# Optimization experiments

Hardware: AMD Instinct MI355X
Metric: run time of the kernel (lower is better)

## Reference

```python
import jax, jax.numpy as jnp
import numpy as np


def setup_inputs() -> dict:
    key = jax.random.key(0)
    ks = jax.random.split(key, 9)
    B, S, H = 4096, 64, 128
    scale = 0.05
    return {
        "feature_input": jax.random.normal(ks[0], (B, S, H), dtype=jnp.float32),
        "W1": jax.random.normal(ks[1], (S, H, H), dtype=jnp.float32) * scale,
        "b1": jax.random.normal(ks[2], (S, H), dtype=jnp.float32) * scale,
        "W3": jax.random.normal(ks[3], (S, H, H), dtype=jnp.float32) * scale,
        "b3": jax.random.normal(ks[4], (S, H), dtype=jnp.float32) * scale,
        "W_ih": jax.random.normal(ks[5], (3 * H, H), dtype=jnp.float32) * scale,
        "b_ih": jax.random.normal(ks[6], (3 * H,), dtype=jnp.float32) * scale,
        "W_hh": jax.random.normal(ks[7], (3 * H, H), dtype=jnp.float32) * scale,
        "b_hh": jax.random.normal(ks[8], (3 * H,), dtype=jnp.float32) * scale,
    }


def _gru_cell(x, h, W_ih, b_ih, W_hh, b_hh):
    # torch.nn.GRUCell math; gate order in weights is (r, z, n)
    gi = x @ W_ih.T + b_ih  # [N, 3H]
    gh = h @ W_hh.T + b_hh  # [N, 3H]
    H = h.shape[-1]
    gi_r, gi_z, gi_n = gi[:, :H], gi[:, H:2 * H], gi[:, 2 * H:]
    gh_r, gh_z, gh_n = gh[:, :H], gh[:, H:2 * H], gh[:, 2 * H:]
    r = jax.nn.sigmoid(gi_r + gh_r)
    z = jax.nn.sigmoid(gi_z + gh_z)
    n = jnp.tanh(gi_n + r * gh_n)
    return (1.0 - z) * n + z * h


def reference(feature_input, W1, b1, W3, b3, W_ih, b_ih, W_hh, b_hh):
    B, S, H = feature_input.shape
    # message pass: per-sen linear (batched over S as one einsum)
    state1 = jnp.einsum('bsh,soh->bso', feature_input, W1) + b1  # [B,S,H]
    # sum over sentences, broadcast-subtract own contribution
    state2 = jnp.sum(state1, axis=1, keepdims=True) - state1      # [B,S,H]
    state3 = jnp.einsum('bsh,soh->bso', state2, W3) + b3          # [B,S,H]
    # GRU cell update over flattened (B*S) nodes
    h_new = _gru_cell(state3.reshape(-1, H), feature_input.reshape(-1, H),
                      W_ih, b_ih, W_hh, b_hh)
    return feature_input + h_new.reshape(B, S, H)
```

## Files before the change

kernel.cpp:

```cpp
#include <hip/hip_runtime.h>
#include <stdint.h>

#define Bdim 4096
#define Sdim 64
#define Hdim 128

typedef __attribute__((ext_vector_type(8))) __bf16 bf16x8;
typedef __attribute__((ext_vector_type(4))) float f32x4;
typedef __attribute__((ext_vector_type(8))) unsigned short ushort8v;

__device__ __forceinline__ unsigned short f2bf(float f) {
  unsigned int u = __float_as_uint(f);
  u = u + 0x7fffu + ((u >> 16) & 1u);
  return (unsigned short)(u >> 16);
}
__device__ __forceinline__ float bf2f(unsigned short s) {
  return __uint_as_float(((unsigned int)s) << 16);
}
__device__ __forceinline__ float sigm(float x) { return 1.0f / (1.0f + __expf(-x)); }
__device__ __forceinline__ float fast_tanh(float x) {
  float t = __expf(-2.0f * fabsf(x));
  float y = (1.0f - t) / (1.0f + t);
  return copysignf(y, x);
}
__device__ __forceinline__ ushort8v pack8(float4 v0, float4 v1) {
  ushort8v o;
  o[0] = f2bf(v0.x); o[1] = f2bf(v0.y); o[2] = f2bf(v0.z); o[3] = f2bf(v0.w);
  o[4] = f2bf(v1.x); o[5] = f2bf(v1.y); o[6] = f2bf(v1.z); o[7] = f2bf(v1.w);
  return o;
}

__device__ __forceinline__ void glds16(const void* g, void* l) {
  auto* gp = reinterpret_cast<__attribute__((address_space(1))) unsigned int*>(
      reinterpret_cast<uintptr_t>(g));
  auto* lp = reinterpret_cast<__attribute__((address_space(3))) unsigned int*>(
      static_cast<uint32_t>(reinterpret_cast<uintptr_t>(l)));
  __builtin_amdgcn_global_load_lds(gp, lp, 16, 0, 0);
}

__device__ __forceinline__ void stage_w(unsigned short* Ws, const unsigned short* wsrc,
                                        int w, int lane) {
#pragma unroll
  for (int i = 0; i < 2; ++i) {
    int chunk = w * 2 + i;
    glds16(wsrc + (size_t)chunk * 512 + lane * 8, Ws + chunk * 512);
  }
}

__device__ __forceinline__ void gemm32(f32x4 acc[2][2], const unsigned short* A,
                                       const unsigned short* W,
                                       const float* __restrict__ biasN,
                                       int wr, int wc, int quad, int l15) {
  const int lane = quad * 16 + l15;
  bf16x8 a[2][4];
#pragma unroll
  for (int rt = 0; rt < 2; ++rt) {
    int row = wr * 32 + rt * 16 + l15;
#pragma unroll
    for (int k0 = 0; k0 < 4; ++k0)
      a[rt][k0] = *(const bf16x8*)&A[row * 128 + (((k0 << 2) | quad) ^ l15) * 8];
  }
#pragma unroll
  for (int ntl = 0; ntl < 2; ++ntl) {
    int nt = wc * 2 + ntl;
    float b = biasN[nt * 16 + l15];
    f32x4 c0 = {b, b, b, b};
    f32x4 c1 = c0;
#pragma unroll
    for (int k0 = 0; k0 < 4; ++k0) {
      bf16x8 bw = *(const bf16x8*)&W[((nt * 4 + k0) * 64 + lane) * 8];
      c0 = __builtin_amdgcn_mfma_f32_16x16x32_bf16(a[0][k0], bw, c0, 0, 0, 0);
      c1 = __builtin_amdgcn_mfma_f32_16x16x32_bf16(a[1][k0], bw, c1, 0, 0, 0);
    }
    acc[0][ntl] = c0;
    acc[1][ntl] = c1;
  }
}

__global__ __launch_bounds__(256) void convert_kernel(
    const float* __restrict__ W1, const float* __restrict__ W3,
    const float* __restrict__ Wih, const float* __restrict__ Whh,
    const float* __restrict__ b1, unsigned short* __restrict__ wsW,
    float* __restrict__ b1s) {
  int cid = blockIdx.x * 256 + threadIdx.x;
  int mat = cid >> 11;
  int within = cid & 2047;
  int f = within >> 6, lane = within & 63;
  int nt = f >> 2, k0 = f & 3;
  int o = nt * 16 + (lane & 15);
  int hb = k0 * 32 + (lane >> 4) * 8;
  const float* src;
  if (mat < 64)       src = W1 + (size_t)mat * 16384;
  else if (mat < 128) src = W3 + (size_t)(mat - 64) * 16384;
  else if (mat < 131) src = Wih + (size_t)(mat - 128) * 16384;
  else                src = Whh + (size_t)(mat - 131) * 16384;
  const float* p = src + o * 128 + hb;
  float4 v0 = *(const float4*)p;
  float4 v1 = *(const float4*)(p + 4);
  *(ushort8v*)(wsW + (size_t)cid * 8) = pack8(v0, v1);
  if (cid < 128) {
    float a = 0.0f;
    for (int s = 0; s < 64; ++s) a += b1[s * 128 + cid];
    b1s[cid] = a;
  }
}

__global__ __launch_bounds__(1024) void sum_kernel(
    const float* __restrict__ X, const unsigned short* __restrict__ wsW1,
    float* __restrict__ sumP) {
  __shared__ unsigned short Xs[2][128 * 128];
  __shared__ unsigned short Ws[2][128 * 128];
  const int t = threadIdx.x;
  const int lane = t & 63, w = t >> 6, quad = lane >> 4, l15 = lane & 15;
  const int wr = w >> 2, wc = w & 3;
  const int m0 = blockIdx.x * 128;
  const int sc = blockIdx.y;
  f32x4 acc[2][2] = {};

  stage_w(Ws[0], wsW1 + (size_t)(sc * 8) * 16384, w, lane);
#pragma unroll
  for (int it = 0; it < 2; ++it) {
    int c = t + it * 1024;
    int r = c >> 4, bblk = c & 15;
    const float* p = X + (size_t)(m0 + r) * 8192 + (sc * 8) * 128 + bblk * 8;
    float4 v0 = *(const float4*)p;
    float4 v1 = *(const float4*)(p + 4);
    *(ushort8v*)(Xs[0] + r * 128 + (bblk ^ (r & 15)) * 8) = pack8(v0, v1);
  }
  __syncthreads();

  for (int si = 0; si < 8; ++si) {
    const int cur = si & 1;
    float4 xr[2][2];
    if (si < 7) {
      int s = sc * 8 + si + 1;
      stage_w(Ws[cur ^ 1], wsW1 + (size_t)s * 16384, w, lane);
#pragma unroll
      for (int it = 0; it < 2; ++it) {
        int c = t + it * 1024;
        int r = c >> 4, bblk = c & 15;
        const float* p = X + (size_t)(m0 + r) * 8192 + s * 128 + bblk * 8;
        xr[it][0] = *(const float4*)p;
        xr[it][1] = *(const float4*)(p + 4);
      }
    }
    {
      bf16x8 a[2][4];
#pragma unroll
      for (int rt = 0; rt < 2; ++rt) {
        int row = wr * 32 + rt * 16 + l15;
#pragma unroll
        for (int k0 = 0; k0 < 4; ++k0)
          a[rt][k0] = *(const bf16x8*)&Xs[cur][row * 128 + (((k0 << 2) | quad) ^ l15) * 8];
      }
#pragma unroll
      for (int ntl = 0; ntl < 2; ++ntl) {
        int nt = wc * 2 + ntl;
#pragma unroll
        for (int k0 = 0; k0 < 4; ++k0) {
          bf16x8 bw = *(const bf16x8*)&Ws[cur][((nt * 4 + k0) * 64 + lane) * 8];
          acc[0][ntl] = __builtin_amdgcn_mfma_f32_16x16x32_bf16(a[0][k0], bw, acc[0][ntl], 0, 0, 0);
          acc[1][ntl] = __builtin_amdgcn_mfma_f32_16x16x32_bf16(a[1][k0], bw, acc[1][ntl], 0, 0, 0);
        }
      }
    }
    if (si < 7) {
#pragma unroll
      for (int it = 0; it < 2; ++it) {
        int c = t + it * 1024;
        int r = c >> 4, bblk = c & 15;
        *(ushort8v*)(Xs[cur ^ 1] + r * 128 + (bblk ^ (r & 15)) * 8) = pack8(xr[it][0], xr[it][1]);
      }
    }
    __syncthreads();
  }
  float* dst = sumP + (size_t)sc * 524288 + (size_t)m0 * 128;
#pragma unroll
  for (int rt = 0; rt < 2; ++rt)
#pragma unroll
    for (int ntl = 0; ntl < 2; ++ntl)
#pragma unroll
      for (int r = 0; r < 4; ++r) {
        int row = wr * 32 + rt * 16 + quad * 4 + r;
        int n = (wc * 2 + ntl) * 16 + l15;
        dst[(size_t)row * 128 + n] = acc[rt][ntl][r];
      }
}

__global__ __launch_bounds__(256) void reduce_kernel(
    const float* __restrict__ sumP, const float* __restrict__ b1s,
    float* __restrict__ sumS) {
  int i = blockIdx.x * 256 + threadIdx.x;
  float4 acc = *(const float4*)(b1s + (i & 31) * 4);
#pragma unroll
  for (int c = 0; c < 8; ++c) {
    float4 v = *(const float4*)(sumP + (size_t)c * 524288 + (size_t)i * 4);
    acc.x += v.x; acc.y += v.y; acc.z += v.z; acc.w += v.w;
  }
  *(float4*)(sumS + (size_t)i * 4) = acc;
}

__global__ __launch_bounds__(1024) void fused_kernel(
    const float* __restrict__ X, const unsigned short* __restrict__ wsW,
    const float* __restrict__ b1, const float* __restrict__ b3,
    const float* __restrict__ bih, const float* __restrict__ bhh,
    const float* __restrict__ sumS, float* __restrict__ out) {
  __shared__ unsigned short Xs[128 * 128];
  __shared__ unsigned short S2[128 * 128];
  __shared__ unsigned short Ws[2][128 * 128];
  const int t = threadIdx.x;
  const int lane = t & 63, w = t >> 6, quad = lane >> 4, l15 = lane & 15;
  const int wr = w >> 2, wc = w & 3;
  const int m0 = blockIdx.x * 128;
  const int s = blockIdx.y;

  const unsigned short* Wptr[8] = {
      wsW + (size_t)s * 16384,
      wsW + (size_t)(64 + s) * 16384,
      wsW + (size_t)128 * 16384,
      wsW + (size_t)131 * 16384,
      wsW + (size_t)129 * 16384,
      wsW + (size_t)132 * 16384,
      wsW + (size_t)130 * 16384,
      wsW + (size_t)133 * 16384};

  stage_w(Ws[0], Wptr[0], w, lane);
#pragma unroll
  for (int it = 0; it < 2; ++it) {
    int c = t + it * 1024;
    int r = c >> 4, bblk = c & 15;
    const float* p = X + (size_t)(m0 + r) * 8192 + s * 128 + bblk * 8;
    float4 v0 = *(const float4*)p;
    float4 v1 = *(const float4*)(p + 4);
    *(ushort8v*)(Xs + r * 128 + (bblk ^ (r & 15)) * 8) = pack8(v0, v1);
  }
  __syncthreads();

  f32x4 gi[2][2], gh[2][2];
  float rg[2][2][4], zg[2][2][4];

  stage_w(Ws[1], Wptr[1], w, lane);
  gemm32(gi, Xs, Ws[0], b1 + s * 128, wr, wc, quad, l15);
  {
    const float* sp = sumS + (size_t)m0 * 128;
#pragma unroll
    for (int rt = 0; rt < 2; ++rt)
#pragma unroll
      for (int ntl = 0; ntl < 2; ++ntl)
#pragma unroll
        for (int r = 0; r < 4; ++r) {
          int rr = quad * 4 + r;
          int row = wr * 32 + rt * 16 + rr;
          int n = (wc * 2 + ntl) * 16 + l15;
          float v = sp[(size_t)row * 128 + n] - gi[rt][ntl][r];
          S2[row * 128 + ((n >> 3) ^ rr) * 8 + (n & 7)] = f2bf(v);
        }
  }
  __syncthreads();
  stage_w(Ws[0], Wptr[2], w, lane);
  gemm32(gi, S2, Ws[1], b3 + s * 128, wr, wc, quad, l15);
  __syncthreads();
#pragma unroll
  for (int rt = 0; rt < 2; ++rt)
#pragma unroll
    for (int ntl = 0; ntl < 2; ++ntl)
#pragma unroll
      for (int r = 0; r < 4; ++r) {
        int rr = quad * 4 + r;
        int row = wr * 32 + rt * 16 + rr;
        int n = (wc * 2 + ntl) * 16 + l15;
        S2[row * 128 + ((n >> 3) ^ rr) * 8 + (n & 7)] = f2bf(gi[rt][ntl][r]);
      }
  __syncthreads();
  stage_w(Ws[1], Wptr[3], w, lane);
  gemm32(gi, S2, Ws[0], bih + 0 * 128, wr, wc, quad, l15);
  __syncthreads();
  stage_w(Ws[0], Wptr[4], w, lane);
  gemm32(gh, Xs, Ws[1], bhh + 0 * 128, wr, wc, quad, l15);
#pragma unroll
  for (int rt = 0; rt < 2; ++rt)
#pragma unroll
    for (int ntl = 0; ntl < 2; ++ntl)
#pragma unroll
      for (int r = 0; r < 4; ++r)
        rg[rt][ntl][r] = sigm(gi[rt][ntl][r] + gh[rt][ntl][r]);
  __syncthreads();
  stage_w(Ws[1], Wptr[5], w, lane);
  gemm32(gi, S2, Ws[0], bih + 1 * 128, wr, wc, quad, l15);
  __syncthreads();
  stage_w(Ws[0], Wptr[6], w, lane);
  gemm32(gh, Xs, Ws[1], bhh + 1 * 128, wr, wc, quad, l15);
#pragma unroll
  for (int rt = 0; rt < 2; ++rt)
#pragma unroll
    for (int ntl = 0; ntl < 2; ++ntl)
#pragma unroll
      for (int r = 0; r < 4; ++r)
        zg[rt][ntl][r] = sigm(gi[rt][ntl][r] + gh[rt][ntl][r]);
  __syncthreads();
  stage_w(Ws[1], Wptr[7], w, lane);
  gemm32(gi, S2, Ws[0], bih + 2 * 128, wr, wc, quad, l15);
  __syncthreads();
  gemm32(gh, Xs, Ws[1], bhh + 2 * 128, wr, wc, quad, l15);
#pragma unroll
  for (int rt = 0; rt < 2; ++rt)
#pragma unroll
    for (int ntl = 0; ntl < 2; ++ntl)
#pragma unroll
      for (int r = 0; r < 4; ++r) {
        int rr = quad * 4 + r;
        int row = wr * 32 + rt * 16 + rr;
        int n = (wc * 2 + ntl) * 16 + l15;
        float nv = fast_tanh(gi[rt][ntl][r] + rg[rt][ntl][r] * gh[rt][ntl][r]);
        float xv = bf2f(Xs[row * 128 + ((n >> 3) ^ rr) * 8 + (n & 7)]);
        float hn = (1.0f - zg[rt][ntl][r]) * nv + zg[rt][ntl][r] * xv;
        out[((size_t)(m0 + row) * 64 + s) * 128 + n] = xv + hn;
      }
}

extern "C" void kernel_launch(void* const* d_in, const int* in_sizes, int n_in,
                              void* d_out, int out_size, void* d_ws, size_t ws_size,
                              hipStream_t stream) {
  const float* X   = (const float*)d_in[0];
  const float* W1  = (const float*)d_in[1];
  const float* b1  = (const float*)d_in[2];
  const float* W3  = (const float*)d_in[3];
  const float* b3  = (const float*)d_in[4];
  const float* Wih = (const float*)d_in[5];
  const float* bih = (const float*)d_in[6];
  const float* Whh = (const float*)d_in[7];
  const float* bhh = (const float*)d_in[8];
  float* out = (float*)d_out;

  const size_t W_BYTES = (size_t)134 * 32768;
  unsigned short* wsW = (unsigned short*)d_ws;
  float* b1s  = (float*)((char*)d_ws + W_BYTES);
  float* sumS = (float*)((char*)d_ws + W_BYTES + 512);
  float* sumP = (float*)((char*)d_ws + W_BYTES + 512 + 2097152);

  convert_kernel<<<1072, 256, 0, stream>>>(W1, W3, Wih, Whh, b1, wsW, b1s);
  sum_kernel<<<dim3(32, 8), 1024, 0, stream>>>(X, wsW, sumP);
  reduce_kernel<<<512, 256, 0, stream>>>(sumP, b1s, sumS);
  fused_kernel<<<dim3(32, 64), 1024, 0, stream>>>(X, wsW, b1, b3, bih, bhh, sumS, out);
}
```

Before: 409.3 us.

## Load GEMM weights straight from global into registers and halve block tile

The fused kernel no longer stages each weight matrix into double-buffered LDS with barriers between GEMMs. Each wave now loads its weight fragments directly from global memory (L2-resident) into registers. The block shrinks to 64 rows and 512 threads with launch bounds for 4 blocks per CU, and a separate S3 buffer removes several __syncthreads. The residual now reads X in fp32 instead of the bf16 copy. The trade-off is repeated global/L2 weight traffic per wave in exchange for less LDS use, fewer barriers and higher occupancy.

Measured after the change: 452.7 us. 1.11x slower.

```diff
diff --git a/kernel.cpp b/kernel.cpp
--- a/kernel.cpp
+++ b/kernel.cpp
@@ -47,33 +47,31 @@
   }
 }
 
-__device__ __forceinline__ void gemm32(f32x4 acc[2][2], const unsigned short* A,
-                                       const unsigned short* W,
+__device__ __forceinline__ void gemm_g(f32x4 acc[2][2], const unsigned short* A,
+                                       const unsigned short* __restrict__ Wg,
                                        const float* __restrict__ biasN,
-                                       int wr, int wc, int quad, int l15) {
-  const int lane = quad * 16 + l15;
-  bf16x8 a[2][4];
-#pragma unroll
-  for (int rt = 0; rt < 2; ++rt) {
-    int row = wr * 32 + rt * 16 + l15;
+                                       int wr, int wc, int quad, int l15, int lane) {
+  bf16x8 bw[2][4];
+#pragma unroll
+  for (int ntl = 0; ntl < 2; ++ntl)
 #pragma unroll
     for (int k0 = 0; k0 < 4; ++k0)
-      a[rt][k0] = *(const bf16x8*)&A[row * 128 + (((k0 << 2) | quad) ^ l15) * 8];
-  }
+      bw[ntl][k0] = *(const bf16x8*)&Wg[(size_t)(((wc * 2 + ntl) * 4 + k0) * 64 + lane) * 8];
 #pragma unroll
   for (int ntl = 0; ntl < 2; ++ntl) {
-    int nt = wc * 2 + ntl;
-    float b = biasN[nt * 16 + l15];
-    f32x4 c0 = {b, b, b, b};
-    f32x4 c1 = c0;
-#pragma unroll
-    for (int k0 = 0; k0 < 4; ++k0) {
-      bf16x8 bw = *(const bf16x8*)&W[((nt * 4 + k0) * 64 + lane) * 8];
-      c0 = __builtin_amdgcn_mfma_f32_16x16x32_bf16(a[0][k0], bw, c0, 0, 0, 0);
-      c1 = __builtin_amdgcn_mfma_f32_16x16x32_bf16(a[1][k0], bw, c1, 0, 0, 0);
+    float b = biasN[(wc * 2 + ntl) * 16 + l15];
+    acc[0][ntl] = (f32x4){b, b, b, b};
+    acc[1][ntl] = acc[0][ntl];
+  }
+#pragma unroll
+  for (int k0 = 0; k0 < 4; ++k0) {
+    bf16x8 a0 = *(const bf16x8*)&A[(wr * 32 + l15) * 128 + (((k0 << 2) | quad) ^ l15) * 8];
+    bf16x8 a1 = *(const bf16x8*)&A[(wr * 32 + 16 + l15) * 128 + (((k0 << 2) | quad) ^ l15) * 8];
+#pragma unroll
+    for (int ntl = 0; ntl < 2; ++ntl) {
+      acc[0][ntl] = __builtin_amdgcn_mfma_f32_16x16x32_bf16(a0, bw[ntl][k0], acc[0][ntl], 0, 0, 0);
+      acc[1][ntl] = __builtin_amdgcn_mfma_f32_16x16x32_bf16(a1, bw[ntl][k0], acc[1][ntl], 0, 0, 0);
     }
-    acc[0][ntl] = c0;
-    acc[1][ntl] = c1;
   }
 }
 
@@ -200,34 +198,28 @@
   *(float4*)(sumS + (size_t)i * 4) = acc;
 }
 
-__global__ __launch_bounds__(1024) void fused_kernel(
+__global__ __launch_bounds__(512, 4) void fused_kernel(
     const float* __restrict__ X, const unsigned short* __restrict__ wsW,
     const float* __restrict__ b1, const float* __restrict__ b3,
     const float* __restrict__ bih, const float* __restrict__ bhh,
     const float* __restrict__ sumS, float* __restrict__ out) {
-  __shared__ unsigned short Xs[128 * 128];
-  __shared__ unsigned short S2[128 * 128];
-  __shared__ unsigned short Ws[2][128 * 128];
+  __shared__ unsigned short Xs[64 * 128];
+  __shared__ unsigned short S2[64 * 128];
+  __shared__ unsigned short S3[64 * 128];
   const int t = threadIdx.x;
   const int lane = t & 63, w = t >> 6, quad = lane >> 4, l15 = lane & 15;
   const int wr = w >> 2, wc = w & 3;
-  const int m0 = blockIdx.x * 128;
+  const int m0 = blockIdx.x * 64;
   const int s = blockIdx.y;
 
-  const unsigned short* Wptr[8] = {
-      wsW + (size_t)s * 16384,
-      wsW + (size_t)(64 + s) * 16384,
-      wsW + (size_t)128 * 16384,
-      wsW + (size_t)131 * 16384,
-      wsW + (size_t)129 * 16384,
-      wsW + (size_t)132 * 16384,
-      wsW + (size_t)130 * 16384,
-      wsW + (size_t)133 * 16384};
-
-  stage_w(Ws[0], Wptr[0], w, lane);
+  const unsigned short* W1g  = wsW + (size_t)s * 16384;
+  const unsigned short* W3g  = wsW + (size_t)(64 + s) * 16384;
+  const unsigned short* Wihg = wsW + (size_t)128 * 16384;
+  const unsigned short* Whhg = wsW + (size_t)131 * 16384;
+
 #pragma unroll
   for (int it = 0; it < 2; ++it) {
-    int c = t + it * 1024;
+    int c = t + it * 512;
     int r = c >> 4, bblk = c & 15;
     const float* p = X + (size_t)(m0 + r) * 8192 + s * 128 + bblk * 8;
     float4 v0 = *(const float4*)p;
@@ -239,27 +231,16 @@
   f32x4 gi[2][2], gh[2][2];
   float rg[2][2][4], zg[2][2][4];
 
-  stage_w(Ws[1], Wptr[1], w, lane);
-  gemm32(gi, Xs, Ws[0], b1 + s * 128, wr, wc, quad, l15);
-  {
-    const float* sp = sumS + (size_t)m0 * 128;
-#pragma unroll
-    for (int rt = 0; rt < 2; ++rt)
-#pragma unroll
-      for (int ntl = 0; ntl < 2; ++ntl)
-#pragma unroll
-        for (int r = 0; r < 4; ++r) {
-          int rr = quad * 4 + r;
-          int row = wr * 32 + rt * 16 + rr;
-          int n = (wc * 2 + ntl) * 16 + l15;
-          float v = sp[(size_t)row * 128 + n] - gi[rt][ntl][r];
-          S2[row * 128 + ((n >> 3) ^ rr) * 8 + (n & 7)] = f2bf(v);
-        }
-  }
-  __syncthreads();
-  stage_w(Ws[0], Wptr[2], w, lane);
-  gemm32(gi, S2, Ws[1], b3 + s * 128, wr, wc, quad, l15);
-  __syncthreads();
+  float sv[2][2][4];
+#pragma unroll
+  for (int rt = 0; rt < 2; ++rt)
+#pragma unroll
+    for (int ntl = 0; ntl < 2; ++ntl)
+#pragma unroll
+      for (int r = 0; r < 4; ++r)
+        sv[rt][ntl][r] = sumS[(size_t)(m0 + wr * 32 + rt * 16 + quad * 4 + r) * 128 +
+                              (wc * 2 + ntl) * 16 + l15];
+  gemm_g(gi, Xs, W1g, b1 + s * 128, wr, wc, quad, l15, lane);
 #pragma unroll
   for (int rt = 0; rt < 2; ++rt)
 #pragma unroll
@@ -269,39 +250,11 @@
         int rr = quad * 4 + r;
         int row = wr * 32 + rt * 16 + rr;
         int n = (wc * 2 + ntl) * 16 + l15;
-        S2[row * 128 + ((n >> 3) ^ rr) * 8 + (n & 7)] = f2bf(gi[rt][ntl][r]);
+        S2[row * 128 + ((n >> 3) ^ rr) * 8 + (n & 7)] = f2bf(sv[rt][ntl][r] - gi[rt][ntl][r]);
       }
   __syncthreads();
-  stage_w(Ws[1], Wptr[3], w, lane);
-  gemm32(gi, S2, Ws[0], bih + 0 * 128, wr, wc, quad, l15);
-  __syncthreads();
-  stage_w(Ws[0], Wptr[4], w, lane);
-  gemm32(gh, Xs, Ws[1], bhh + 0 * 128, wr, wc, quad, l15);
-#pragma unroll
-  for (int rt = 0; rt < 2; ++rt)
-#pragma unroll
-    for (int ntl = 0; ntl < 2; ++ntl)
-#pragma unroll
-      for (int r = 0; r < 4; ++r)
-        rg[rt][ntl][r] = sigm(gi[rt][ntl][r] + gh[rt][ntl][r]);
-  __syncthreads();
-  stage_w(Ws[1], Wptr[5], w, lane);
-  gemm32(gi, S2, Ws[0], bih + 1 * 128, wr, wc, quad, l15);
-  __syncthreads();
-  stage_w(Ws[0], Wptr[6], w, lane);
-  gemm32(gh, Xs, Ws[1], bhh + 1 * 128, wr, wc, quad, l15);
-#pragma unroll
-  for (int rt = 0; rt < 2; ++rt)
-#pragma unroll
-    for (int ntl = 0; ntl < 2; ++ntl)
-#pragma unroll
-      for (int r = 0; r < 4; ++r)
-        zg[rt][ntl][r] = sigm(gi[rt][ntl][r] + gh[rt][ntl][r]);
-  __syncthreads();
-  stage_w(Ws[1], Wptr[7], w, lane);
-  gemm32(gi, S2, Ws[0], bih + 2 * 128, wr, wc, quad, l15);
-  __syncthreads();
-  gemm32(gh, Xs, Ws[1], bhh + 2 * 128, wr, wc, quad, l15);
+
+  gemm_g(gi, S2, W3g, b3 + s * 128, wr, wc, quad, l15, lane);
 #pragma unroll
   for (int rt = 0; rt < 2; ++rt)
 #pragma unroll
@@ -311,8 +264,43 @@
         int rr = quad * 4 + r;
         int row = wr * 32 + rt * 16 + rr;
         int n = (wc * 2 + ntl) * 16 + l15;
+        S3[row * 128 + ((n >> 3) ^ rr) * 8 + (n & 7)] = f2bf(gi[rt][ntl][r]);
+      }
+  __syncthreads();
+
+  gemm_g(gi, S3, Wihg + 0 * 16384, bih + 0 * 128, wr, wc, quad, l15, lane);
+  gemm_g(gh, Xs, Whhg + 0 * 16384, bhh + 0 * 128, wr, wc, quad, l15, lane);
+#pragma unroll
+  for (int rt = 0; rt < 2; ++rt)
+#pragma unroll
+    for (int ntl = 0; ntl < 2; ++ntl)
+#pragma unroll
+      for (int r = 0; r < 4; ++r)
+        rg[rt][ntl][r] = sigm(gi[rt][ntl][r] + gh[rt][ntl][r]);
+
+  gemm_g(gi, S3, Wihg + 1 * 16384, bih + 1 * 128, wr, wc, quad, l15, lane);
+  gemm_g(gh, Xs, Whhg + 1 * 16384, bhh + 1 * 128, wr, wc, quad, l15, lane);
+#pragma unroll
+  for (int rt = 0; rt < 2; ++rt)
+#pragma unroll
+    for (int ntl = 0; ntl < 2; ++ntl)
+#pragma unroll
+      for (int r = 0; r < 4; ++r)
+        zg[rt][ntl][r] = sigm(gi[rt][ntl][r] + gh[rt][ntl][r]);
+
+  gemm_g(gi, S3, Wihg + 2 * 16384, bih + 2 * 128, wr, wc, quad, l15, lane);
+  gemm_g(gh, Xs, Whhg + 2 * 16384, bhh + 2 * 128, wr, wc, quad, l15, lane);
+#pragma unroll
+  for (int rt = 0; rt < 2; ++rt)
+#pragma unroll
+    for (int ntl = 0; ntl < 2; ++ntl)
+#pragma unroll
+      for (int r = 0; r < 4; ++r) {
+        int rr = quad * 4 + r;
+        int row = wr * 32 + rt * 16 + rr;
+        int n = (wc * 2 + ntl) * 16 + l15;
+        float xv = X[(size_t)(m0 + row) * 8192 + s * 128 + n];
         float nv = fast_tanh(gi[rt][ntl][r] + rg[rt][ntl][r] * gh[rt][ntl][r]);
-        float xv = bf2f(Xs[row * 128 + ((n >> 3) ^ rr) * 8 + (n & 7)]);
         float hn = (1.0f - zg[rt][ntl][r]) * nv + zg[rt][ntl][r] * xv;
         out[((size_t)(m0 + row) * 64 + s) * 128 + n] = xv + hn;
       }
@@ -341,5 +329,5 @@
   convert_kernel<<<1072, 256, 0, stream>>>(W1, W3, Wih, Whh, b1, wsW, b1s);
   sum_kernel<<<dim3(32, 8), 1024, 0, stream>>>(X, wsW, sumP);
   reduce_kernel<<<512, 256, 0, stream>>>(sumP, b1s, sumS);
-  fused_kernel<<<dim3(32, 64), 1024, 0, stream>>>(X, wsW, b1, b3, bih, bhh, sumS, out);
-}
+  fused_kernel<<<dim3(64, 64), 512, 0, stream>>>(X, wsW, b1, b3, bih, bhh, sumS, out);
+}
```

## Cache bf16 swizzled X from sum kernel and reuse A fragments in fused kernel

Applied to the files above, without the earlier changes.

The sum kernel now also writes the bf16-converted, pre-swizzled X tiles to a workspace buffer. The fused kernel loads those tiles straight into LDS with global_load_lds instead of reading fp32 X and converting it. It also keeps the A-operand fragments for X and state3 in registers across the three GRU gate GEMMs, instead of reloading them from LDS for each gate. This halves the X read traffic in the main kernel at the cost of an extra 64MB bf16 write in sum_kernel plus higher register pressure. A fallback path remains for when the workspace is too small.

Result: slower. 442.3 us (+8.1%).

```diff
diff --git a/kernel.cpp b/kernel.cpp
--- a/kernel.cpp
+++ b/kernel.cpp
@@ -47,12 +47,8 @@
   }
 }
 
-__device__ __forceinline__ void gemm32(f32x4 acc[2][2], const unsigned short* A,
-                                       const unsigned short* W,
-                                       const float* __restrict__ biasN,
-                                       int wr, int wc, int quad, int l15) {
-  const int lane = quad * 16 + l15;
-  bf16x8 a[2][4];
+__device__ __forceinline__ void load_a(bf16x8 a[2][4], const unsigned short* A,
+                                       int wr, int quad, int l15) {
 #pragma unroll
   for (int rt = 0; rt < 2; ++rt) {
     int row = wr * 32 + rt * 16 + l15;
@@ -60,6 +56,12 @@
     for (int k0 = 0; k0 < 4; ++k0)
       a[rt][k0] = *(const bf16x8*)&A[row * 128 + (((k0 << 2) | quad) ^ l15) * 8];
   }
+}
+
+__device__ __forceinline__ void gemm_ws(f32x4 acc[2][2], const bf16x8 a[2][4],
+                                        const unsigned short* Ws,
+                                        const float* __restrict__ biasN,
+                                        int wc, int l15, int lane) {
 #pragma unroll
   for (int ntl = 0; ntl < 2; ++ntl) {
     int nt = wc * 2 + ntl;
@@ -68,7 +70,7 @@
     f32x4 c1 = c0;
 #pragma unroll
     for (int k0 = 0; k0 < 4; ++k0) {
-      bf16x8 bw = *(const bf16x8*)&W[((nt * 4 + k0) * 64 + lane) * 8];
+      bf16x8 bw = *(const bf16x8*)&Ws[((nt * 4 + k0) * 64 + lane) * 8];
       c0 = __builtin_amdgcn_mfma_f32_16x16x32_bf16(a[0][k0], bw, c0, 0, 0, 0);
       c1 = __builtin_amdgcn_mfma_f32_16x16x32_bf16(a[1][k0], bw, c1, 0, 0, 0);
     }
@@ -107,13 +109,14 @@
 
 __global__ __launch_bounds__(1024) void sum_kernel(
     const float* __restrict__ X, const unsigned short* __restrict__ wsW1,
-    float* __restrict__ sumP) {
+    float* __restrict__ sumP, unsigned short* __restrict__ xbf) {
   __shared__ unsigned short Xs[2][128 * 128];
   __shared__ unsigned short Ws[2][128 * 128];
   const int t = threadIdx.x;
   const int lane = t & 63, w = t >> 6, quad = lane >> 4, l15 = lane & 15;
   const int wr = w >> 2, wc = w & 3;
-  const int m0 = blockIdx.x * 128;
+  const int mi = blockIdx.x;
+  const int m0 = mi * 128;
   const int sc = blockIdx.y;
   f32x4 acc[2][2] = {};
 
@@ -125,7 +128,10 @@
     const float* p = X + (size_t)(m0 + r) * 8192 + (sc * 8) * 128 + bblk * 8;
     float4 v0 = *(const float4*)p;
     float4 v1 = *(const float4*)(p + 4);
-    *(ushort8v*)(Xs[0] + r * 128 + (bblk ^ (r & 15)) * 8) = pack8(v0, v1);
+    ushort8v o = pack8(v0, v1);
+    int off = r * 128 + (bblk ^ (r & 15)) * 8;
+    *(ushort8v*)(Xs[0] + off) = o;
+    if (xbf) *(ushort8v*)(xbf + ((size_t)mi * 64 + sc * 8) * 16384 + off) = o;
   }
   __syncthreads();
 
@@ -146,13 +152,7 @@
     }
     {
       bf16x8 a[2][4];
-#pragma unroll
-      for (int rt = 0; rt < 2; ++rt) {
-        int row = wr * 32 + rt * 16 + l15;
-#pragma unroll
-        for (int k0 = 0; k0 < 4; ++k0)
-          a[rt][k0] = *(const bf16x8*)&Xs[cur][row * 128 + (((k0 << 2) | quad) ^ l15) * 8];
-      }
+      load_a(a, Xs[cur], wr, quad, l15);
 #pragma unroll
       for (int ntl = 0; ntl < 2; ++ntl) {
         int nt = wc * 2 + ntl;
@@ -165,11 +165,15 @@
       }
     }
     if (si < 7) {
+      int s = sc * 8 + si + 1;
 #pragma unroll
       for (int it = 0; it < 2; ++it) {
         int c = t + it * 1024;
         int r = c >> 4, bblk = c & 15;
-        *(ushort8v*)(Xs[cur ^ 1] + r * 128 + (bblk ^ (r & 15)) * 8) = pack8(xr[it][0], xr[it][1]);
+        ushort8v o = pack8(xr[it][0], xr[it][1]);
+        int off = r * 128 + (bblk ^ (r & 15)) * 8;
+        *(ushort8v*)(Xs[cur ^ 1] + off) = o;
+        if (xbf) *(ushort8v*)(xbf + ((size_t)mi * 64 + s) * 16384 + off) = o;
       }
     }
     __syncthreads();
@@ -200,7 +204,137 @@
   *(float4*)(sumS + (size_t)i * 4) = acc;
 }
 
-__global__ __launch_bounds__(1024) void fused_kernel(
+__global__ __launch_bounds__(1024, 4) void fused_kernel(
+    const unsigned short* __restrict__ Xbf, const unsigned short* __restrict__ wsW,
+    const float* __restrict__ b1, const float* __restrict__ b3,
+    const float* __restrict__ bih, const float* __restrict__ bhh,
+    const float* __restrict__ sumS, float* __restrict__ out) {
+  __shared__ unsigned short Xs[128 * 128];
+  __shared__ unsigned short S23[128 * 128];
+  __shared__ unsigned short Ws[2][128 * 128];
+  const int t = threadIdx.x;
+  const int lane = t & 63, w = t >> 6, quad = lane >> 4, l15 = lane & 15;
+  const int wr = w >> 2, wc = w & 3;
+  const int m0 = blockIdx.x * 128;
+  const int s = blockIdx.y;
+
+  const unsigned short* Wp_W1  = wsW + (size_t)s * 16384;
+  const unsigned short* Wp_W3  = wsW + (size_t)(64 + s) * 16384;
+  const unsigned short* Wp_ihr = wsW + (size_t)128 * 16384;
+  const unsigned short* Wp_ihz = wsW + (size_t)129 * 16384;
+  const unsigned short* Wp_ihn = wsW + (size_t)130 * 16384;
+  const unsigned short* Wp_hhr = wsW + (size_t)131 * 16384;
+  const unsigned short* Wp_hhz = wsW + (size_t)132 * 16384;
+  const unsigned short* Wp_hhn = wsW + (size_t)133 * 16384;
+
+  stage_w(Ws[0], Wp_W1, w, lane);
+  stage_w(Xs, Xbf + ((size_t)blockIdx.x * 64 + s) * 16384, w, lane);
+  __syncthreads();
+
+  bf16x8 xa[2][4];
+  load_a(xa, Xs, wr, quad, l15);
+
+  f32x4 t0[2][2];
+  stage_w(Ws[1], Wp_W3, w, lane);
+  {
+    float sv[2][2][4];
+#pragma unroll
+    for (int rt = 0; rt < 2; ++rt)
+#pragma unroll
+      for (int ntl = 0; ntl < 2; ++ntl)
+#pragma unroll
+        for (int r = 0; r < 4; ++r)
+          sv[rt][ntl][r] = sumS[(size_t)(m0 + wr * 32 + rt * 16 + quad * 4 + r) * 128 +
+                                (wc * 2 + ntl) * 16 + l15];
+    gemm_ws(t0, xa, Ws[0], b1 + s * 128, wc, l15, lane);
+#pragma unroll
+    for (int rt = 0; rt < 2; ++rt)
+#pragma unroll
+      for (int ntl = 0; ntl < 2; ++ntl)
+#pragma unroll
+        for (int r = 0; r < 4; ++r) {
+          int rr = quad * 4 + r;
+          int row = wr * 32 + rt * 16 + rr;
+          int n = (wc * 2 + ntl) * 16 + l15;
+          S23[row * 128 + ((n >> 3) ^ rr) * 8 + (n & 7)] = f2bf(sv[rt][ntl][r] - t0[rt][ntl][r]);
+        }
+  }
+  __syncthreads();
+
+  stage_w(Ws[0], Wp_ihr, w, lane);
+  {
+    bf16x8 s2a[2][4];
+    load_a(s2a, S23, wr, quad, l15);
+    gemm_ws(t0, s2a, Ws[1], b3 + s * 128, wc, l15, lane);
+  }
+  __syncthreads();
+#pragma unroll
+  for (int rt = 0; rt < 2; ++rt)
+#pragma unroll
+    for (int ntl = 0; ntl < 2; ++ntl)
+#pragma unroll
+      for (int r = 0; r < 4; ++r) {
+        int rr = quad * 4 + r;
+        int row = wr * 32 + rt * 16 + rr;
+        int n = (wc * 2 + ntl) * 16 + l15;
+        S23[row * 128 + ((n >> 3) ^ rr) * 8 + (n & 7)] = f2bf(t0[rt][ntl][r]);
+      }
+  __syncthreads();
+
+  bf16x8 s3a[2][4];
+  load_a(s3a, S23, wr, quad, l15);
+
+  f32x4 gir[2][2], giz[2][2], gin[2][2], gh[2][2];
+
+  stage_w(Ws[1], Wp_ihz, w, lane);
+  gemm_ws(gir, s3a, Ws[0], bih + 0 * 128, wc, l15, lane);
+  __syncthreads();
+  stage_w(Ws[0], Wp_ihn, w, lane);
+  gemm_ws(giz, s3a, Ws[1], bih + 1 * 128, wc, l15, lane);
+  __syncthreads();
+  stage_w(Ws[1], Wp_hhr, w, lane);
+  gemm_ws(gin, s3a, Ws[0], bih + 2 * 128, wc, l15, lane);
+  __syncthreads();
+
+  float rg[2][2][4], zg[2][2][4];
+  stage_w(Ws[0], Wp_hhz, w, lane);
+  gemm_ws(gh, xa, Ws[1], bhh + 0 * 128, wc, l15, lane);
+#pragma unroll
+  for (int rt = 0; rt < 2; ++rt)
+#pragma unroll
+    for (int ntl = 0; ntl < 2; ++ntl)
+#pragma unroll
+      for (int r = 0; r < 4; ++r)
+        rg[rt][ntl][r] = sigm(gir[rt][ntl][r] + gh[rt][ntl][r]);
+  __syncthreads();
+  stage_w(Ws[1], Wp_hhn, w, lane);
+  gemm_ws(gh, xa, Ws[0], bhh + 1 * 128, wc, l15, lane);
+#pragma unroll
+  for (int rt = 0; rt < 2; ++rt)
+#pragma unroll
+    for (int ntl = 0; ntl < 2; ++ntl)
+#pragma unroll
+      for (int r = 0; r < 4; ++r)
+        zg[rt][ntl][r] = sigm(giz[rt][ntl][r] + gh[rt][ntl][r]);
+  __syncthreads();
+  gemm_ws(gh, xa, Ws[1], bhh + 2 * 128, wc, l15, lane);
+#pragma unroll
+  for (int rt = 0; rt < 2; ++rt)
+#pragma unroll
+    for (int ntl = 0; ntl < 2; ++ntl)
+#pragma unroll
+      for (int r = 0; r < 4; ++r) {
+        int rr = quad * 4 + r;
+        int row = wr * 32 + rt * 16 + rr;
+        int n = (wc * 2 + ntl) * 16 + l15;
+        float nv = fast_tanh(gin[rt][ntl][r] + rg[rt][ntl][r] * gh[rt][ntl][r]);
+        float xv = bf2f(Xs[row * 128 + ((n >> 3) ^ rr) * 8 + (n & 7)]);
+        float hn = (1.0f - zg[rt][ntl][r]) * nv + zg[rt][ntl][r] * xv;
+        out[((size_t)(m0 + row) * 64 + s) * 128 + n] = xv + hn;
+      }
+}
+
+__global__ __launch_bounds__(1024) void fused_kernel_fb(
     const float* __restrict__ X, const unsigned short* __restrict__ wsW,
     const float* __restrict__ b1, const float* __restrict__ b3,
     const float* __restrict__ bih, const float* __restrict__ bhh,
@@ -215,14 +349,10 @@
   const int s = blockIdx.y;
 
   const unsigned short* Wptr[8] = {
-      wsW + (size_t)s * 16384,
-      wsW + (size_t)(64 + s) * 16384,
-      wsW + (size_t)128 * 16384,
-      wsW + (size_t)131 * 16384,
-      wsW + (size_t)129 * 16384,
-      wsW + (size_t)132 * 16384,
-      wsW + (size_t)130 * 16384,
-      wsW + (size_t)133 * 16384};
+      wsW + (size_t)s * 16384,          wsW + (size_t)(64 + s) * 16384,
+      wsW + (size_t)128 * 16384,        wsW + (size_t)131 * 16384,
+      wsW + (size_t)129 * 16384,        wsW + (size_t)132 * 16384,
+      wsW + (size_t)130 * 16384,        wsW + (size_t)133 * 16384};
 
   stage_w(Ws[0], Wptr[0], w, lane);
 #pragma unroll
@@ -240,7 +370,11 @@
   float rg[2][2][4], zg[2][2][4];
 
   stage_w(Ws[1], Wptr[1], w, lane);
-  gemm32(gi, Xs, Ws[0], b1 + s * 128, wr, wc, quad, l15);
+  {
+    bf16x8 a[2][4];
+    load_a(a, Xs, wr, quad, l15);
+    gemm_ws(gi, a, Ws[0], b1 + s * 128, wc, l15, lane);
+  }
   {
     const float* sp = sumS + (size_t)m0 * 128;
 #pragma unroll
@@ -258,7 +392,11 @@
   }
   __syncthreads();
   stage_w(Ws[0], Wptr[2], w, lane);
-  gemm32(gi, S2, Ws[1], b3 + s * 128, wr, wc, quad, l15);
+  {
+    bf16x8 a[2][4];
+    load_a(a, S2, wr, quad, l15);
+    gemm_ws(gi, a, Ws[1], b3 + s * 128, wc, l15, lane);
+  }
   __syncthreads();
 #pragma unroll
   for (int rt = 0; rt < 2; ++rt)
@@ -273,10 +411,18 @@
       }
   __syncthreads();
   stage_w(Ws[1], Wptr[3], w, lane);
-  gemm32(gi, S2, Ws[0], bih + 0 * 128, wr, wc, quad, l15);
+  {
+    bf16x8 a[2][4];
+    load_a(a, S2, wr, quad, l15);
+    gemm_ws(gi, a, Ws[0], bih + 0 * 128, wc, l15, lane);
+  }
   __syncthreads();
   stage_w(Ws[0], Wptr[4], w, lane);
-  gemm32(gh, Xs, Ws[1], bhh + 0 * 128, wr, wc, quad, l15);
+  {
+    bf16x8 a[2][4];
+    load_a(a, Xs, wr, quad, l15);
+    gemm_ws(gh, a, Ws[1], bhh + 0 * 128, wc, l15, lane);
+  }
 #pragma unroll
   for (int rt = 0; rt < 2; ++rt)
 #pragma unroll
@@ -286,10 +432,18 @@
         rg[rt][ntl][r] = sigm(gi[rt][ntl][r] + gh[rt][ntl][r]);
   __syncthreads();
   stage_w(Ws[1], Wptr[5], w, lane);
-  gemm32(gi, S2, Ws[0], bih + 1 * 128, wr, wc, quad, l15);
+  {
+    bf16x8 a[2][4];
+    load_a(a, S2, wr, quad, l15);
+    gemm_ws(gi, a, Ws[0], bih + 1 * 128, wc, l15, lane);
+  }
   __syncthreads();
   stage_w(Ws[0], Wptr[6], w, lane);
-  gemm32(gh, Xs, Ws[1], bhh + 1 * 128, wr, wc, quad, l15);
+  {
+    bf16x8 a[2][4];
+    load_a(a, Xs, wr, quad, l15);
+    gemm_ws(gh, a, Ws[1], bhh + 1 * 128, wc, l15, lane);
+  }
 #pragma unroll
   for (int rt = 0; rt < 2; ++rt)
 #pragma unroll
@@ -299,9 +453,17 @@
         zg[rt][ntl][r] = sigm(gi[rt][ntl][r] + gh[rt][ntl][r]);
   __syncthreads();
   stage_w(Ws[1], Wptr[7], w, lane);
-  gemm32(gi, S2, Ws[0], bih + 2 * 128, wr, wc, quad, l15);
-  __syncthreads();
-  gemm32(gh, Xs, Ws[1], bhh + 2 * 128, wr, wc, quad, l15);
+  {
+    bf16x8 a[2][4];
+    load_a(a, S2, wr, quad, l15);
+    gemm_ws(gi, a, Ws[0], bih + 2 * 128, wc, l15, lane);
+  }
+  __syncthreads();
+  {
+    bf16x8 a[2][4];
+    load_a(a, Xs, wr, quad, l15);
+    gemm_ws(gh, a, Ws[1], bhh + 2 * 128, wc, l15, lane);
+  }
 #pragma unroll
   for (int rt = 0; rt < 2; ++rt)
 #pragma unroll
@@ -332,14 +494,21 @@
   const float* bhh = (const float*)d_in[8];
   float* out = (float*)d_out;
 
-  const size_t W_BYTES = (size_t)134 * 32768;
+  const size_t W_BYTES  = (size_t)134 * 32768;
+  const size_t XBF_OFF  = W_BYTES + 512 + 2097152 + 16777216;
+  const size_t XBF_SZ   = (size_t)4096 * 8192 * 2;
   unsigned short* wsW = (unsigned short*)d_ws;
   float* b1s  = (float*)((char*)d_ws + W_BYTES);
   float* sumS = (float*)((char*)d_ws + W_BYTES + 512);
   float* sumP = (float*)((char*)d_ws + W_BYTES + 512 + 2097152);
+  const bool fast = ws_size >= XBF_OFF + XBF_SZ;
+  unsigned short* xbf = fast ? (unsigned short*)((char*)d_ws + XBF_OFF) : nullptr;
 
   convert_kernel<<<1072, 256, 0, stream>>>(W1, W3, Wih, Whh, b1, wsW, b1s);
-  sum_kernel<<<dim3(32, 8), 1024, 0, stream>>>(X, wsW, sumP);
+  sum_kernel<<<dim3(32, 8), 1024, 0, stream>>>(X, wsW, sumP, xbf);
   reduce_kernel<<<512, 256, 0, stream>>>(sumP, b1s, sumS);
-  fused_kernel<<<dim3(32, 64), 1024, 0, stream>>>(X, wsW, b1, b3, bih, bhh, sumS, out);
-}
+  if (fast)
+    fused_kernel<<<dim3(32, 64), 1024, 0, stream>>>(xbf, wsW, b1, b3, bih, bhh, sumS, out);
+  else
+    fused_kernel_fb<<<dim3(32, 64), 1024, 0, stream>>>(X, wsW, b1, b3, bih, bhh, sumS, out);
+}
```
